# Kernel optimization log

Hardware: AMD Instinct MI355X
Metric: run time of the kernel (lower is better)

## Reference

```python
import jax, jax.numpy as jnp
import numpy as np

B, T, D, R, V, L, QK, H = 8, 1024, 768, 768, 768, 13, 32, 4
HEAD_DIM = QK // H  # 8
TEMPERATURE = 2.0
LN_EPS = 1e-5


def _layernorm(x, g, b):
    m = jnp.mean(x, axis=-1, keepdims=True)
    v = jnp.mean(jnp.square(x - m), axis=-1, keepdims=True)
    return (x - m) * jax.lax.rsqrt(v + LN_EPS) * g + b


def setup_inputs() -> dict:
    key = jax.random.key(0)
    ks = jax.random.split(key, 14)
    s = 0.02
    return {
        "base_hidden_state": jax.random.normal(ks[0], (B, T, D), jnp.float32),
        "layer_reps": jax.random.normal(ks[1], (L, B, T, R), jnp.float32),
        # per-layer aligner Linear(R -> V)
        "aligner_w": jax.random.normal(ks[2], (L, V, R), jnp.float32) * s,
        "aligner_b": jax.random.normal(ks[3], (L, V), jnp.float32) * s,
        # query LayerNorm(D)
        "qln_g": jnp.ones((D,), jnp.float32),
        "qln_b": jnp.zeros((D,), jnp.float32),
        # kv LayerNorm(V)
        "kvln_g": jnp.ones((V,), jnp.float32),
        "kvln_b": jnp.zeros((V,), jnp.float32),
        # q_proj: D -> QK ; k_proj: V -> QK
        "q_w": jax.random.normal(ks[4], (QK, D), jnp.float32) * s,
        "q_b": jax.random.normal(ks[5], (QK,), jnp.float32) * s,
        "k_w": jax.random.normal(ks[6], (QK, V), jnp.float32) * s,
        "k_b": jax.random.normal(ks[7], (QK,), jnp.float32) * s,
        # out_proj: H*V -> D
        "out_w": jax.random.normal(ks[8], (D, H * V), jnp.float32) * s,
        "out_b": jax.random.normal(ks[9], (D,), jnp.float32) * s,
    }


def reference(base_hidden_state, layer_reps, aligner_w, aligner_b,
              qln_g, qln_b, kvln_g, kvln_b, q_w, q_b, k_w, k_b, out_w, out_b):
    # align_representations: per-layer Linear(R->V), stacked -> (B,T,L,V)
    aligned = jnp.einsum('lbtr,lvr->btlv', layer_reps, aligner_w) + aligner_b  # (B,T,L,V)
    # query: LN of final hidden state (Tq = 1 per token)
    Q = _layernorm(base_hidden_state, qln_g, qln_b)           # (B,T,D)
    # K and V share the same LayerNorm output
    KV = _layernorm(aligned, kvln_g, kvln_b)                  # (B,T,L,V)
    # low-dim projections
    q = jnp.einsum('btd,qd->btq', Q, q_w) + q_b               # (B,T,QK)
    k = jnp.einsum('btlv,qv->btlq', KV, k_w) + k_b            # (B,T,L,QK)
    qh = q.reshape(B, T, H, HEAD_DIM)                         # (B,T,H,hd)
    kh = k.reshape(B, T, L, H, HEAD_DIM)                      # (B,T,L,H,hd)
    scale = HEAD_DIM ** 0.5
    scores = jnp.einsum('bthd,btlhd->bthl', qh, kh) / scale / TEMPERATURE  # (B,T,H,L)
    scores = jnp.where(jnp.isnan(scores), -jnp.inf, scores)
    attn = jax.nn.softmax(scores, axis=-1)                    # (B,T,H,L)
    # V is NOT projected: each head attends over the full-dim values
    out_heads = jnp.einsum('bthl,btlv->bthv', attn, KV)       # (B,T,H,V)
    out = jnp.einsum('bthv,dx->btd', out_heads.reshape(B, T, H * V)[..., None, :].squeeze(-2)[..., None, :].squeeze(-2).reshape(B, T, H * V), out_w.reshape(D, H * V).T.reshape(H * V, D)) if False else out_heads.reshape(B, T, H * V) @ out_w.T + out_b  # (B,T,D)
    return out
```

## Files before the change

### kernel.cpp

```cpp
#include <hip/hip_runtime.h>
#include <stdint.h>

#define NB 8
#define NT 1024
#define ND 768
#define NV 768
#define NL 13
#define MTOK (NB*NT)
#define MROWS (MTOK*NL)

typedef __attribute__((ext_vector_type(8))) short short8;
typedef __attribute__((ext_vector_type(4))) float f32x4;

__device__ __forceinline__ unsigned short f2bf(float f) {
    union { float f; unsigned u; } v; v.f = f;
    unsigned r = v.u + 0x7FFFu + ((v.u >> 16) & 1u);
    return (unsigned short)(r >> 16);
}
__device__ __forceinline__ float bf2f(unsigned short u) {
    union { unsigned u; float f; } v; v.u = ((unsigned)u) << 16;
    return v.f;
}
__device__ __forceinline__ unsigned cvtpk(float lo, float hi) {
    unsigned r;
    asm("v_cvt_pk_bf16_f32 %0, %1, %2" : "=v"(r) : "v"(lo), "v"(hi));
    return r;
}
__device__ __forceinline__ void gload16(const void* g, void* l) {
    __builtin_amdgcn_global_load_lds(
        (const __attribute__((address_space(1))) unsigned int*)g,
        (__attribute__((address_space(3))) unsigned int*)l, 16, 0, 0);
}

__global__ __launch_bounds__(256) void conv_f32_bf16(
    const float* __restrict__ s, unsigned short* __restrict__ d, long n)
{
    long i = ((long)blockIdx.x * 256 + threadIdx.x) * 8;
    long st = (long)gridDim.x * 2048;
    for (; i < n; i += st) {
        float4 a = *(const float4*)(s + i);
        float4 b = *(const float4*)(s + i + 4);
        ushort4 u0, u1;
        u0.x = f2bf(a.x); u0.y = f2bf(a.y); u0.z = f2bf(a.z); u0.w = f2bf(a.w);
        u1.x = f2bf(b.x); u1.y = f2bf(b.y); u1.z = f2bf(b.z); u1.w = f2bf(b.w);
        *(ushort4*)(d + i)     = u0;
        *(ushort4*)(d + i + 4) = u1;
    }
}

__global__ __launch_bounds__(256) void gemm_f32a(
    const float* __restrict__ A, const unsigned short* __restrict__ B,
    const float* __restrict__ biasBase, unsigned short* __restrict__ C,
    int K, long aLS, long bLS, int biasLS, long cLayerOff, long cRowStride)
{
    __shared__ __align__(16) float          lsA[2][4096];
    __shared__ __align__(16) unsigned short lsB[2][4096];

    const int bid = blockIdx.x;
    const int xcd = bid & 7, slot = bid >> 3;
    const int grp = xcd * 104 + slot / 6;
    const int nx  = slot % 6;
    const int l   = grp >> 6;
    const long m0 = (long)(grp & 63) * 128;
    const long n0 = (long)nx * 128;

    const int t = threadIdx.x, lane = t & 63, wave = t >> 6;

    const float* Ab = A + (size_t)l * aLS;
    const unsigned short* Bb = B + (size_t)l * bLS;
    const float* bias = biasBase + (size_t)l * biasLS;

    const int arow = wave * 8 + (lane >> 3);
    const int achk = (lane & 7) ^ (lane >> 3);
    const int brow = wave * 16 + (lane >> 2);
    const int bchk = (lane & 3) ^ ((lane >> 3) & 3);
    const int dA   = wave * 1024 + lane * 16;

    const int wm = (wave >> 1) * 64;
    const int wn = (wave & 1) * 64;
    const int lr = lane & 15;
    const int g4 = lane >> 4;
    const int kg = g4 * 8;
    const int swzB = ((lr >> 1) & 3) * 8;

    f32x4 acc[4][4];
#pragma unroll
    for (int i = 0; i < 4; i++)
#pragma unroll
        for (int j = 0; j < 4; j++) acc[i][j] = (f32x4){0.f, 0.f, 0.f, 0.f};

    auto STAGE = [&](int buf, int k0) {
        char* la = (char*)lsA[buf];
        char* lb = (char*)lsB[buf];
#pragma unroll
        for (int i = 0; i < 4; i++) {
            const char* src = (const char*)(Ab + (m0 + i * 32 + arow) * (size_t)K + k0) + achk * 16;
            gload16(src, la + i * 4096 + dA);
        }
#pragma unroll
        for (int i = 0; i < 2; i++) {
            const char* src = (const char*)(Bb + (n0 + i * 64 + brow) * (size_t)K + k0) + bchk * 16;
            gload16(src, lb + i * 4096 + dA);
        }
    };
    auto COMP = [&](int buf) {
        short8 af[4], bv[4];
        const float* pa = lsA[buf];
        const unsigned short* pb = lsB[buf];
#pragma unroll
        for (int mi = 0; mi < 4; mi++) {
            int row = wm + mi * 16 + lr;
            const char* base = (const char*)(pa + row * 32);
            float4 x0 = *(const float4*)(base + (((2 * g4 + 0) ^ (row & 7)) << 4));
            float4 x1 = *(const float4*)(base + (((2 * g4 + 1) ^ (row & 7)) << 4));
            union { short8 s; unsigned u[4]; } ua;
            ua.u[0] = cvtpk(x0.x, x0.y); ua.u[1] = cvtpk(x0.z, x0.w);
            ua.u[2] = cvtpk(x1.x, x1.y); ua.u[3] = cvtpk(x1.z, x1.w);
            af[mi] = ua.s;
        }
#pragma unroll
        for (int ni = 0; ni < 4; ni++)
            bv[ni] = *(const short8*)&pb[(wn + ni * 16 + lr) * 32 + (kg ^ swzB)];
#pragma unroll
        for (int mi = 0; mi < 4; mi++)
#pragma unroll
            for (int ni = 0; ni < 4; ni++)
                acc[mi][ni] = __builtin_amdgcn_mfma_f32_16x16x32_bf16(
                    af[mi], bv[ni], acc[mi][ni], 0, 0, 0);
    };

    STAGE(0, 0);
    __syncthreads();
    int cur = 0;
    const int nst = K >> 5;
    for (int ks = 1; ks < nst; ks++) {
        STAGE(cur ^ 1, ks * 32);
        COMP(cur);
        __syncthreads();
        cur ^= 1;
    }
    COMP(cur);

#pragma unroll
    for (int ni = 0; ni < 4; ni++) {
        long col = n0 + wn + ni * 16 + lr;
        float bvs = bias[col];
#pragma unroll
        for (int mi = 0; mi < 4; mi++) {
#pragma unroll
            for (int r = 0; r < 4; r++) {
                long grow = m0 + wm + mi * 16 + (lane >> 4) * 4 + r;
                size_t coff = (size_t)grow * cRowStride + (size_t)l * cLayerOff + col;
                C[coff] = f2bf(acc[mi][ni][r] + bvs);
            }
        }
    }
}

__global__ __launch_bounds__(256) void gemm_bf16_nt(
    const unsigned short* __restrict__ A, const unsigned short* __restrict__ B,
    const float* __restrict__ bias, float* __restrict__ C,
    int K, long cRowStride)
{
    __shared__ __align__(16) unsigned short lsA[2][4096];
    __shared__ __align__(16) unsigned short lsB[2][4096];

    const int bid = blockIdx.x;
    const int xcd = bid & 7, slot = bid >> 3;
    const int grp = xcd * 8 + slot / 6;
    const int nx  = slot % 6;
    const long m0 = (long)grp * 128;
    const long n0 = (long)nx * 128;

    const int t = threadIdx.x, lane = t & 63, wave = t >> 6;

    const int brow = wave * 16 + (lane >> 2);
    const int bchk = (lane & 3) ^ ((lane >> 3) & 3);
    const int dA   = wave * 1024 + lane * 16;

    const int wm = (wave >> 1) * 64;
    const int wn = (wave & 1) * 64;
    const int lr = lane & 15;
    const int g4 = lane >> 4;
    const int kg = g4 * 8;
    const int swz = ((lr >> 1) & 3) * 8;

    f32x4 acc[4][4];
#pragma unroll
    for (int i = 0; i < 4; i++)
#pragma unroll
        for (int j = 0; j < 4; j++) acc[i][j] = (f32x4){0.f, 0.f, 0.f, 0.f};

    auto STAGE = [&](int buf, int k0) {
        char* la = (char*)lsA[buf];
        char* lb = (char*)lsB[buf];
#pragma unroll
        for (int i = 0; i < 2; i++) {
            const char* sa = (const char*)(A + (m0 + i * 64 + brow) * (size_t)K + k0) + bchk * 16;
            const char* sb = (const char*)(B + (n0 + i * 64 + brow) * (size_t)K + k0) + bchk * 16;
            gload16(sa, la + i * 4096 + dA);
            gload16(sb, lb + i * 4096 + dA);
        }
    };
    auto COMP = [&](int buf) {
        short8 af[4], bv[4];
        const unsigned short* pa = lsA[buf];
        const unsigned short* pb = lsB[buf];
#pragma unroll
        for (int mi = 0; mi < 4; mi++)
            af[mi] = *(const short8*)&pa[(wm + mi * 16 + lr) * 32 + (kg ^ swz)];
#pragma unroll
        for (int ni = 0; ni < 4; ni++)
            bv[ni] = *(const short8*)&pb[(wn + ni * 16 + lr) * 32 + (kg ^ swz)];
#pragma unroll
        for (int mi = 0; mi < 4; mi++)
#pragma unroll
            for (int ni = 0; ni < 4; ni++)
                acc[mi][ni] = __builtin_amdgcn_mfma_f32_16x16x32_bf16(
                    af[mi], bv[ni], acc[mi][ni], 0, 0, 0);
    };

    STAGE(0, 0);
    __syncthreads();
    int cur = 0;
    const int nst = K >> 5;
    for (int ks = 1; ks < nst; ks++) {
        STAGE(cur ^ 1, ks * 32);
        COMP(cur);
        __syncthreads();
        cur ^= 1;
    }
    COMP(cur);

#pragma unroll
    for (int ni = 0; ni < 4; ni++) {
        long col = n0 + wn + ni * 16 + lr;
        float bvs = bias[col];
#pragma unroll
        for (int mi = 0; mi < 4; mi++) {
#pragma unroll
            for (int r = 0; r < 4; r++) {
                long grow = m0 + wm + mi * 16 + (lane >> 4) * 4 + r;
                C[(size_t)grow * cRowStride + col] = acc[mi][ni][r] + bvs;
            }
        }
    }
}

__global__ __launch_bounds__(256) void wtrans(
    const float* __restrict__ kw, const float* __restrict__ kvg,
    const float* __restrict__ kvb, const float* __restrict__ kbias,
    float* __restrict__ kwp, float* __restrict__ skv, float* __restrict__ ckv)
{
    __shared__ float red[8];
    const int q = blockIdx.x, t = threadIdx.x;
    const int lane = t & 63, wave = t >> 6;
    float s = 0.f, c = 0.f;
    for (int v = t; v < 768; v += 256) {
        float w = kw[q * 768 + v];
        float wp = w * kvg[v];
        kwp[q * 768 + v] = wp;
        s += wp;
        c += w * kvb[v];
    }
#pragma unroll
    for (int off = 1; off < 64; off <<= 1) {
        s += __shfl_xor(s, off);
        c += __shfl_xor(c, off);
    }
    if (lane == 0) { red[wave] = s; red[4 + wave] = c; }
    __syncthreads();
    if (t == 0) {
        skv[q] = red[0] + red[1] + red[2] + red[3];
        ckv[q] = red[4] + red[5] + red[6] + red[7] + kbias[q];
    }
}

__global__ __launch_bounds__(256) void ln_rows_f32(
    const float* __restrict__ src, unsigned short* __restrict__ dst,
    const float* __restrict__ gam, const float* __restrict__ bet)
{
    const int lane = threadIdx.x & 63;
    const int wave = threadIdx.x >> 6;
    const size_t row = (size_t)blockIdx.x * 4 + wave;

    float x[3][4];
    float s = 0.f, sq = 0.f;
#pragma unroll
    for (int i = 0; i < 3; i++) {
        int v = i * 256 + lane * 4;
        float4 f = *(const float4*)(src + row * 768 + v);
        x[i][0] = f.x; x[i][1] = f.y; x[i][2] = f.z; x[i][3] = f.w;
#pragma unroll
        for (int e = 0; e < 4; e++) { s += x[i][e]; sq += x[i][e] * x[i][e]; }
    }
#pragma unroll
    for (int off = 1; off < 64; off <<= 1) {
        s  += __shfl_xor(s, off);
        sq += __shfl_xor(sq, off);
    }
    float mean = s * (1.f / 768.f);
    float var  = sq * (1.f / 768.f) - mean * mean;
    float rs   = rsqrtf(var + 1e-5f);
#pragma unroll
    for (int i = 0; i < 3; i++) {
        int v = i * 256 + lane * 4;
        float4 gg = *(const float4*)(gam + v);
        float4 bb = *(const float4*)(bet + v);
        ushort4 o;
        o.x = f2bf((x[i][0] - mean) * rs * gg.x + bb.x);
        o.y = f2bf((x[i][1] - mean) * rs * gg.y + bb.y);
        o.z = f2bf((x[i][2] - mean) * rs * gg.z + bb.z);
        o.w = f2bf((x[i][3] - mean) * rs * gg.w + bb.w);
        *(ushort4*)(dst + row * 768 + v) = o;
    }
}

__global__ __launch_bounds__(256) void proj32(
    const unsigned short* __restrict__ A, const float* __restrict__ W,
    const float* __restrict__ bias, unsigned short* __restrict__ out)
{
    __shared__ __align__(16) unsigned short lsW[32 * 776];
    __shared__ __align__(16) unsigned short lsA[128 * 40];
    const int t = threadIdx.x;

#pragma unroll
    for (int i = 0; i < 24; i++) {
        int fi = t + i * 256;
        int row = fi / 192;
        int c4  = fi % 192;
        float4 f = *(const float4*)(W + row * 768 + c4 * 4);
        ushort4 u;
        u.x = f2bf(f.x); u.y = f2bf(f.y); u.z = f2bf(f.z); u.w = f2bf(f.w);
        *(ushort4*)&lsW[row * 776 + c4 * 4] = u;
    }

    const size_t m0 = (size_t)blockIdx.x * 128;
    const int lane = t & 63, wave = t >> 6;
    const int wm = wave * 32;
    const int lr = lane & 15, kg = (lane >> 4) * 8;
    const int row_s = t >> 3, c4s = t & 7;

    f32x4 acc[2][2];
#pragma unroll
    for (int i = 0; i < 2; i++)
#pragma unroll
        for (int j = 0; j < 2; j++) acc[i][j] = (f32x4){0.f, 0.f, 0.f, 0.f};

    __syncthreads();

    for (int k0 = 0; k0 < 768; k0 += 32) {
#pragma unroll
        for (int i = 0; i < 4; i++) {
            int row = row_s + 32 * i;
            ushort4 v = *(const ushort4*)(A + (m0 + row) * 768 + k0 + c4s * 4);
            *(ushort4*)&lsA[row * 40 + c4s * 4] = v;
        }
        __syncthreads();
        short8 af[2], bw[2];
#pragma unroll
        for (int mi = 0; mi < 2; mi++)
            af[mi] = *(const short8*)&lsA[(wm + mi * 16 + lr) * 40 + kg];
#pragma unroll
        for (int ni = 0; ni < 2; ni++)
            bw[ni] = *(const short8*)&lsW[(ni * 16 + lr) * 776 + k0 + kg];
#pragma unroll
        for (int mi = 0; mi < 2; mi++)
#pragma unroll
            for (int ni = 0; ni < 2; ni++)
                acc[mi][ni] = __builtin_amdgcn_mfma_f32_16x16x32_bf16(
                    af[mi], bw[ni], acc[mi][ni], 0, 0, 0);
        __syncthreads();
    }

#pragma unroll
    for (int ni = 0; ni < 2; ni++) {
        int col = ni * 16 + lr;
        float bv = bias[col];
#pragma unroll
        for (int mi = 0; mi < 2; mi++) {
#pragma unroll
            for (int r = 0; r < 4; r++) {
                size_t grow = m0 + wm + mi * 16 + (lane >> 4) * 4 + r;
                out[grow * 32 + col] = f2bf(acc[mi][ni][r] + bv);
            }
        }
    }
}

__global__ __launch_bounds__(256) void proj32k_stats(
    const unsigned short* __restrict__ A, const float* __restrict__ W,
    const float* __restrict__ skv, const float* __restrict__ ckv,
    unsigned short* __restrict__ out, float2* __restrict__ st)
{
    __shared__ __align__(16) unsigned short lsW[32 * 776];
    __shared__ __align__(16) unsigned short lsA[128 * 40];
    __shared__ float2 lstat[128];
    const int t = threadIdx.x;

#pragma unroll
    for (int i = 0; i < 24; i++) {
        int fi = t + i * 256;
        int row = fi / 192;
        int c4  = fi % 192;
        float4 f = *(const float4*)(W + row * 768 + c4 * 4);
        ushort4 u;
        u.x = f2bf(f.x); u.y = f2bf(f.y); u.z = f2bf(f.z); u.w = f2bf(f.w);
        *(ushort4*)&lsW[row * 776 + c4 * 4] = u;
    }

    const size_t m0 = (size_t)blockIdx.x * 128;
    const int lane = t & 63, wave = t >> 6;
    const int wm = wave * 32;
    const int lr = lane & 15, kg = (lane >> 4) * 8;
    const int row_s = t >> 3, c4s = t & 7;

    f32x4 acc[2][2];
#pragma unroll
    for (int i = 0; i < 2; i++)
#pragma unroll
        for (int j = 0; j < 2; j++) acc[i][j] = (f32x4){0.f, 0.f, 0.f, 0.f};

    float s_[4] = {0.f, 0.f, 0.f, 0.f}, sq_[4] = {0.f, 0.f, 0.f, 0.f};

    __syncthreads();

    for (int k0 = 0; k0 < 768; k0 += 32) {
#pragma unroll
        for (int i = 0; i < 4; i++) {
            int row = row_s + 32 * i;
            ushort4 v = *(const ushort4*)(A + (m0 + row) * 768 + k0 + c4s * 4);
            *(ushort4*)&lsA[row * 40 + c4s * 4] = v;
            float x0 = bf2f(v.x), x1 = bf2f(v.y), x2 = bf2f(v.z), x3 = bf2f(v.w);
            s_[i]  += x0 + x1 + x2 + x3;
            sq_[i] += x0 * x0 + x1 * x1 + x2 * x2 + x3 * x3;
        }
        __syncthreads();
        short8 af[2], bw[2];
#pragma unroll
        for (int mi = 0; mi < 2; mi++)
            af[mi] = *(const short8*)&lsA[(wm + mi * 16 + lr) * 40 + kg];
#pragma unroll
        for (int ni = 0; ni < 2; ni++)
            bw[ni] = *(const short8*)&lsW[(ni * 16 + lr) * 776 + k0 + kg];
#pragma unroll
        for (int mi = 0; mi < 2; mi++)
#pragma unroll
            for (int ni = 0; ni < 2; ni++)
                acc[mi][ni] = __builtin_amdgcn_mfma_f32_16x16x32_bf16(
                    af[mi], bw[ni], acc[mi][ni], 0, 0, 0);
        __syncthreads();
    }

#pragma unroll
    for (int i = 0; i < 4; i++) {
#pragma unroll
        for (int off = 1; off < 8; off <<= 1) {
            s_[i]  += __shfl_xor(s_[i], off);
            sq_[i] += __shfl_xor(sq_[i], off);
        }
    }
    if (c4s == 0) {
#pragma unroll
        for (int i = 0; i < 4; i++) {
            int row = row_s + 32 * i;
            float mean = s_[i] * (1.f / 768.f);
            float var  = sq_[i] * (1.f / 768.f) - mean * mean;
            float2 sv = make_float2(mean, rsqrtf(var + 1e-5f));
            lstat[row] = sv;
            st[m0 + row] = sv;
        }
    }
    __syncthreads();

#pragma unroll
    for (int ni = 0; ni < 2; ni++) {
        int col = ni * 16 + lr;
        float sk = skv[col], ck = ckv[col];
#pragma unroll
        for (int mi = 0; mi < 2; mi++) {
#pragma unroll
            for (int r = 0; r < 4; r++) {
                int lrow = wm + mi * 16 + (lane >> 4) * 4 + r;
                float2 s2 = lstat[lrow];
                out[(m0 + lrow) * 32 + col] =
                    f2bf(s2.y * (acc[mi][ni][r] - s2.x * sk) + ck);
            }
        }
    }
}

__global__ __launch_bounds__(256) void attn2(
    const unsigned short* __restrict__ qb, const unsigned short* __restrict__ kb,
    const unsigned short* __restrict__ kv, const float2* __restrict__ st,
    const float* __restrict__ gv, const float* __restrict__ bvv,
    unsigned short* __restrict__ oh)
{
    __shared__ float lat[4][4][13];
    __shared__ float latc[4][4];
    const int t = threadIdx.x, lane = t & 63, wave = t >> 6;
    const size_t m = (size_t)blockIdx.x * 4 + wave;

    if (lane < 32) {
        int j = lane;
        float qv = bf2f(qb[m * 32 + j]);
        float p[13];
#pragma unroll
        for (int l = 0; l < 13; l++)
            p[l] = qv * bf2f(kb[(m * 13 + l) * 32 + j]);
#pragma unroll
        for (int off = 1; off < 8; off <<= 1)
#pragma unroll
            for (int l = 0; l < 13; l++) p[l] += __shfl_xor(p[l], off);

        const float sc = 0.17677669529663687f;
        float mx = -1e30f;
#pragma unroll
        for (int l = 0; l < 13; l++) { p[l] *= sc; mx = fmaxf(mx, p[l]); }
        float se = 0.f;
#pragma unroll
        for (int l = 0; l < 13; l++) { p[l] = __expf(p[l] - mx); se += p[l]; }
        float inv = 1.f / se;
        if ((j & 7) == 0) {
            int h = j >> 3;
            float corr = 0.f;
#pragma unroll
            for (int l = 0; l < 13; l++) {
                float2 s_ = st[m * 13 + l];
                float wl = p[l] * inv * s_.y;
                lat[wave][h][l] = wl;
                corr += wl * s_.x;
            }
            latc[wave][h] = corr;
        }
    }
    __syncthreads();

    f32x4 g4v[3], b4[3];
#pragma unroll
    for (int i = 0; i < 3; i++) {
        g4v[i] = *(const f32x4*)(gv + i * 256 + lane * 4);
        b4[i] = *(const f32x4*)(bvv + i * 256 + lane * 4);
    }

    float acc[4][3][4];
#pragma unroll
    for (int h = 0; h < 4; h++)
#pragma unroll
        for (int i = 0; i < 3; i++)
#pragma unroll
            for (int e = 0; e < 4; e++) acc[h][i][e] = 0.f;

    for (int l = 0; l < 13; l++) {
        float al[4];
#pragma unroll
        for (int h = 0; h < 4; h++) al[h] = lat[wave][h][l];
#pragma unroll
        for (int i = 0; i < 3; i++) {
            ushort4 u = *(const ushort4*)(kv + (m * 13 + l) * 768 + i * 256 + lane * 4);
            float xv[4] = {bf2f(u.x), bf2f(u.y), bf2f(u.z), bf2f(u.w)};
#pragma unroll
            for (int h = 0; h < 4; h++)
#pragma unroll
                for (int e = 0; e < 4; e++) acc[h][i][e] += al[h] * xv[e];
        }
    }
#pragma unroll
    for (int h = 0; h < 4; h++) {
        float ch = latc[wave][h];
#pragma unroll
        for (int i = 0; i < 3; i++) {
            ushort4 o;
            o.x = f2bf(g4v[i][0] * (acc[h][i][0] - ch) + b4[i][0]);
            o.y = f2bf(g4v[i][1] * (acc[h][i][1] - ch) + b4[i][1]);
            o.z = f2bf(g4v[i][2] * (acc[h][i][2] - ch) + b4[i][2]);
            o.w = f2bf(g4v[i][3] * (acc[h][i][3] - ch) + b4[i][3]);
            *(ushort4*)(oh + m * 3072 + h * 768 + i * 256 + lane * 4) = o;
        }
    }
}

extern "C" void kernel_launch(void* const* d_in, const int* in_sizes, int n_in,
                              void* d_out, int out_size, void* d_ws, size_t ws_size,
                              hipStream_t stream) {
    const float* base  = (const float*)d_in[0];
    const float* reps  = (const float*)d_in[1];
    const float* aw    = (const float*)d_in[2];
    const float* ab    = (const float*)d_in[3];
    const float* qg    = (const float*)d_in[4];
    const float* qbeta = (const float*)d_in[5];
    const float* kvg   = (const float*)d_in[6];
    const float* kvb   = (const float*)d_in[7];
    const float* qw    = (const float*)d_in[8];
    const float* qbias = (const float*)d_in[9];
    const float* kw    = (const float*)d_in[10];
    const float* kbias = (const float*)d_in[11];
    const float* ow    = (const float*)d_in[12];
    const float* obias = (const float*)d_in[13];
    float* out = (float*)d_out;

    float2* stats = (float2*)d_ws;
    float* kwp = (float*)(stats + MROWS);
    float* skv = kwp + 32 * 768;
    float* ckv = skv + 32;
    unsigned short* aligned = (unsigned short*)(ckv + 32);
    unsigned short* UNION = aligned + (size_t)MROWS * 768;
    unsigned short* kbuf = UNION + (size_t)MTOK * 3072;
    unsigned short* qbuf = kbuf + (size_t)MROWS * 32;
    unsigned short* owb  = qbuf + (size_t)MTOK * 32;

    unsigned short* awb = UNION;

    {
        long n = (long)NL * 768 * 768;
        conv_f32_bf16<<<(int)(n / 8 / 256), 256, 0, stream>>>(aw, awb, n);
        long n2 = (long)768 * 3072;
        conv_f32_bf16<<<(int)(n2 / 8 / 256), 256, 0, stream>>>(ow, owb, n2);
        wtrans<<<32, 256, 0, stream>>>(kw, kvg, kvb, kbias, kwp, skv, ckv);
    }

    gemm_f32a<<<4992, 256, 0, stream>>>(
        reps, awb, ab, aligned,
        768, (long)MTOK * 768, (long)768 * 768, 768,
        768L, (long)NL * 768);

    proj32k_stats<<<MROWS / 128, 256, 0, stream>>>(
        aligned, kwp, skv, ckv, kbuf, stats);

    unsigned short* Qn = UNION;
    ln_rows_f32<<<MTOK / 4, 256, 0, stream>>>(base, Qn, qg, qbeta);
    proj32<<<MTOK / 128, 256, 0, stream>>>(Qn, qw, qbias, qbuf);

    unsigned short* oh = UNION;
    attn2<<<MTOK / 4, 256, 0, stream>>>(qbuf, kbuf, aligned, stats, kvg, kvb, oh);

    gemm_bf16_nt<<<384, 256, 0, stream>>>(oh, owb, obias, out, 3072, 768L);
}
```

Before: 464.3 us.

## Convert A tile to bf16 in registers before LDS, padded layout

The fp32 A operand was staged into LDS with direct global-to-LDS loads and converted to bf16 by every wave on each LDS read. Now each thread loads its A slice into registers, converts it once, and writes bf16 into a padded (stride 40) LDS tile after the compute step. This halves the A footprint in LDS, removes the repeated conversions in the inner loop, and overlaps global loads with MFMA work. In exchange it adds register pressure and a VGPR round trip instead of async direct-to-LDS loads, and the padded layout may still cause some bank conflicts.

```diff
diff --git a/kernel.cpp b/kernel.cpp
--- a/kernel.cpp
+++ b/kernel.cpp
@@ -53,7 +53,7 @@
     const float* __restrict__ biasBase, unsigned short* __restrict__ C,
     int K, long aLS, long bLS, int biasLS, long cLayerOff, long cRowStride)
 {
-    __shared__ __align__(16) float          lsA[2][4096];
+    __shared__ __align__(16) unsigned short lsA[2][128 * 40];
     __shared__ __align__(16) unsigned short lsB[2][4096];
 
     const int bid = blockIdx.x;
@@ -70,11 +70,11 @@
     const unsigned short* Bb = B + (size_t)l * bLS;
     const float* bias = biasBase + (size_t)l * biasLS;
 
-    const int arow = wave * 8 + (lane >> 3);
-    const int achk = (lane & 7) ^ (lane >> 3);
+    const int aRow = t >> 3;
+    const int aChk = t & 7;
     const int brow = wave * 16 + (lane >> 2);
     const int bchk = (lane & 3) ^ ((lane >> 3) & 3);
-    const int dA   = wave * 1024 + lane * 16;
+    const int dB   = wave * 1024 + lane * 16;
 
     const int wm = (wave >> 1) * 64;
     const int wn = (wave & 1) * 64;
@@ -89,35 +89,38 @@
 #pragma unroll
         for (int j = 0; j < 4; j++) acc[i][j] = (f32x4){0.f, 0.f, 0.f, 0.f};
 
-    auto STAGE = [&](int buf, int k0) {
-        char* la = (char*)lsA[buf];
+    f32x4 areg[4];
+
+    auto LOAD_A = [&](int k0) {
+#pragma unroll
+        for (int i = 0; i < 4; i++)
+            areg[i] = *(const f32x4*)(Ab + (m0 + aRow + i * 32) * (size_t)K + k0 + aChk * 4);
+    };
+    auto WRITE_A = [&](int buf) {
+        unsigned short* la = lsA[buf];
+#pragma unroll
+        for (int i = 0; i < 4; i++) {
+            unsigned u0 = cvtpk(areg[i][0], areg[i][1]);
+            unsigned u1 = cvtpk(areg[i][2], areg[i][3]);
+            uint2 w; w.x = u0; w.y = u1;
+            *(uint2*)&la[(aRow + i * 32) * 40 + aChk * 4] = w;
+        }
+    };
+    auto STAGE_B = [&](int buf, int k0) {
         char* lb = (char*)lsB[buf];
-#pragma unroll
-        for (int i = 0; i < 4; i++) {
-            const char* src = (const char*)(Ab + (m0 + i * 32 + arow) * (size_t)K + k0) + achk * 16;
-            gload16(src, la + i * 4096 + dA);
-        }
 #pragma unroll
         for (int i = 0; i < 2; i++) {
             const char* src = (const char*)(Bb + (n0 + i * 64 + brow) * (size_t)K + k0) + bchk * 16;
-            gload16(src, lb + i * 4096 + dA);
+            gload16(src, lb + i * 4096 + dB);
         }
     };
     auto COMP = [&](int buf) {
         short8 af[4], bv[4];
-        const float* pa = lsA[buf];
+        const unsigned short* pa = lsA[buf];
         const unsigned short* pb = lsB[buf];
 #pragma unroll
-        for (int mi = 0; mi < 4; mi++) {
-            int row = wm + mi * 16 + lr;
-            const char* base = (const char*)(pa + row * 32);
-            float4 x0 = *(const float4*)(base + (((2 * g4 + 0) ^ (row & 7)) << 4));
-            float4 x1 = *(const float4*)(base + (((2 * g4 + 1) ^ (row & 7)) << 4));
-            union { short8 s; unsigned u[4]; } ua;
-            ua.u[0] = cvtpk(x0.x, x0.y); ua.u[1] = cvtpk(x0.z, x0.w);
-            ua.u[2] = cvtpk(x1.x, x1.y); ua.u[3] = cvtpk(x1.z, x1.w);
-            af[mi] = ua.s;
-        }
+        for (int mi = 0; mi < 4; mi++)
+            af[mi] = *(const short8*)&pa[(wm + mi * 16 + lr) * 40 + kg];
 #pragma unroll
         for (int ni = 0; ni < 4; ni++)
             bv[ni] = *(const short8*)&pb[(wn + ni * 16 + lr) * 32 + (kg ^ swzB)];
@@ -129,13 +132,17 @@
                     af[mi], bv[ni], acc[mi][ni], 0, 0, 0);
     };
 
-    STAGE(0, 0);
+    LOAD_A(0);
+    STAGE_B(0, 0);
+    WRITE_A(0);
     __syncthreads();
     int cur = 0;
     const int nst = K >> 5;
     for (int ks = 1; ks < nst; ks++) {
-        STAGE(cur ^ 1, ks * 32);
+        LOAD_A(ks * 32);
+        STAGE_B(cur ^ 1, ks * 32);
         COMP(cur);
+        WRITE_A(cur ^ 1);
         __syncthreads();
         cur ^= 1;
     }
```

After: 467.0 us. Within noise of the previous version (+0.6%).
